# Optimization experiments

Hardware: AMD Instinct MI355X
Metric: run time of the kernel (lower is better)

## Reference

```python
import jax, jax.numpy as jnp
import numpy as np

L, B, S, D, H = 6, 2, 2048, 512, 8
DH = D // H
FF = 4 * D
EPS = 1e-5


def setup_inputs() -> dict:
    key = jax.random.key(0)
    ks = jax.random.split(key, 10)
    w = lambda k, shape: jax.random.normal(k, shape, jnp.float32) * 0.02
    return {
        "query": jax.random.normal(ks[0], (B, S, D), jnp.float32),
        "key": jax.random.normal(ks[1], (B, S, D), jnp.float32),
        "query_mask": jnp.ones((B, S), jnp.int32),
        "key_mask": jnp.ones((B, S), jnp.int32),
        # per-layer stacked params; conv1d(kernel=1) == linear with weight [out,in]
        "Wq": w(ks[2], (L, D, D)), "bq": jnp.zeros((L, D), jnp.float32),
        "Wk": w(ks[3], (L, D, D)), "bk": jnp.zeros((L, D), jnp.float32),
        "Wv": w(ks[4], (L, D, D)), "bv": jnp.zeros((L, D), jnp.float32),
        "Wo": w(ks[5], (L, D, D)), "bo": jnp.zeros((L, D), jnp.float32),
        "ln1_g": jnp.ones((L, D), jnp.float32), "ln1_b": jnp.zeros((L, D), jnp.float32),
        "ff_w1": w(ks[6], (L, FF, D)), "ff_b1": jnp.zeros((L, FF), jnp.float32),
        "ff_w2": w(ks[7], (L, D, FF)), "ff_b2": jnp.zeros((L, D), jnp.float32),
        "ln2_g": jnp.ones((L, D), jnp.float32), "ln2_b": jnp.zeros((L, D), jnp.float32),
    }


def _layer_norm(x, g, b):
    m = jnp.mean(x, axis=-1, keepdims=True)
    v = jnp.mean(jnp.square(x - m), axis=-1, keepdims=True)
    return (x - m) * jax.lax.rsqrt(v + EPS) * g + b


def reference(query, key, query_mask, key_mask,
              Wq, bq, Wk, bk, Wv, bv, Wo, bo,
              ln1_g, ln1_b, ff_w1, ff_b1, ff_w2, ff_b2, ln2_g, ln2_b):
    b_, s_, d_ = query.shape
    kpad = (key_mask == 0)[:, None, None, :]          # [B,1,1,K]
    qm = query_mask.astype(query.dtype)[:, :, None]    # [B,S,1]
    x = query
    for i in range(L):
        # QKV projections (conv1d kernel-size-1 == linear), split heads -> [B,H,S,DH]
        def split(t):
            return t.reshape(b_, s_, H, DH).transpose(0, 2, 1, 3)
        q = split(x @ Wq[i].T + bq[i]) * (float(DH) ** -0.5)
        k = split(key @ Wk[i].T + bk[i])
        v = split(key @ Wv[i].T + bv[i])
        attn = jnp.einsum('bhqd,bhkd->bhqk', q, k)
        attn = jnp.where(kpad, -jnp.inf, attn)
        attn = jax.nn.softmax(attn, axis=-1)
        o = jnp.einsum('bhqk,bhkd->bhqd', attn, v)
        o = o.transpose(0, 2, 1, 3).reshape(b_, s_, H * DH)
        o = (o @ Wo[i].T + bo[i]) * qm                 # output proj + query mask
        x = _layer_norm(o + x, ln1_g[i], ln1_b[i])
        h = jax.nn.leaky_relu(x @ ff_w1[i].T + ff_b1[i], 0.01)
        f = (h @ ff_w2[i].T + ff_b2[i]) * qm           # FFN mask on output
        x = _layer_norm(f + x, ln2_g[i], ln2_b[i])
    return x
```

## Files before the change

kernel.cpp:

```cpp
#include <hip/hip_runtime.h>
#include <stdint.h>

constexpr int LAYERS = 6;
constexpr int Bc = 2, Sc = 2048, Dc = 512, Hc = 8, DHc = 64, FFc = 2048;
constexpr int Mc = Bc * Sc;
constexpr int NS = 2;
constexpr int KCHUNK = Sc / NS;

typedef __attribute__((ext_vector_type(8))) __bf16 bf16x8;
typedef __attribute__((ext_vector_type(4))) __bf16 bf16x4;
typedef __attribute__((ext_vector_type(4))) float f32x4;

__device__ __forceinline__ void async_ld16(const void* g, void* lds) {
  __builtin_amdgcn_global_load_lds(
      (const __attribute__((address_space(1))) uint32_t*)g,
      (__attribute__((address_space(3))) uint32_t*)lds, 16, 0, 0);
}

__global__ __launch_bounds__(256) void cvt_kernel(const float* __restrict__ in,
                                                  __bf16* __restrict__ out, int n) {
  int i = (blockIdx.x * 256 + threadIdx.x) * 4;
  if (i + 4 > n) return;
  const float4 v = *(const float4*)(in + i);
  bf16x4 o;
  o[0] = (__bf16)v.x; o[1] = (__bf16)v.y; o[2] = (__bf16)v.z; o[3] = (__bf16)v.w;
  *(bf16x4*)(out + i) = o;
}

__global__ __launch_bounds__(256) void cvt_kv_kernel(const float* __restrict__ Wk,
                                                     const float* __restrict__ Wv,
                                                     __bf16* __restrict__ out) {
  size_t i = ((size_t)blockIdx.x * 256 + threadIdx.x) * 4;
  int n = (int)(i / ((size_t)Dc * Dc));
  int lyr = n >> 1, p = n & 1;
  size_t idx = i - (size_t)n * Dc * Dc;
  const float* src = (p ? Wv : Wk) + (size_t)lyr * Dc * Dc + idx;
  const float4 v = *(const float4*)src;
  bf16x4 o;
  o[0] = (__bf16)v.x; o[1] = (__bf16)v.y; o[2] = (__bf16)v.z; o[3] = (__bf16)v.w;
  *(bf16x4*)(out + i) = o;
}

__global__ __launch_bounds__(256) void kbias_kernel(const int* __restrict__ km,
                                                    float* __restrict__ kb, int n) {
  int i = blockIdx.x * 256 + threadIdx.x;
  if (i < n) kb[i] = km[i] ? 0.f : -1e30f;
}

template <int BM, int BN, int WM, int WN, int EPI>
__global__ __launch_bounds__(256) void gemm_bt(
    const __bf16* __restrict__ A, const __bf16* __restrict__ W,
    const float* __restrict__ bias, const float* __restrict__ bias2,
    float* __restrict__ outf, __bf16* __restrict__ outb,
    __bf16* __restrict__ outb2, float scale,
    int M, int N, int K, int Kstride) {
  constexpr int BK = 64;
  __shared__ __bf16 As[2][BM * BK];
  __shared__ __bf16 Bs[2][BN * BK];
  const int tid = threadIdx.x;
  const int l15 = tid & 15;
  const int lg = (tid & 63) >> 4;
  const int w = tid >> 6;
  const int wm = w >> 1, wn = w & 1;
  const int tm = blockIdx.y * BM;
  const int tn = blockIdx.x * BN;
  const int z = blockIdx.z;
  const __bf16* Ap = A + (size_t)tm * Kstride + (size_t)z * K;
  const __bf16* Wp = W + (size_t)tn * Kstride + (size_t)z * K;
  f32x4 acc[WM][WN] = {};

  auto stage = [&](int k0, int bf) {
#pragma unroll
    for (int c = 0; c < BM * 8 / 256; ++c) {
      int cc = c * 256 + tid;
      int r = cc >> 3, s = cc & 7;
      int ss = s ^ (r & 7);
      async_ld16(Ap + (size_t)r * Kstride + k0 + ss * 8, &As[bf][cc * 8]);
    }
#pragma unroll
    for (int c = 0; c < BN * 8 / 256; ++c) {
      int cc = c * 256 + tid;
      int r = cc >> 3, s = cc & 7;
      int ss = s ^ (r & 7);
      async_ld16(Wp + (size_t)r * Kstride + k0 + ss * 8, &Bs[bf][cc * 8]);
    }
  };

  const int nk = K / BK;
  stage(0, 0);
  __syncthreads();
  int buf = 0;
  for (int t = 0; t < nk; ++t) {
    if (t + 1 < nk) stage((t + 1) * BK, buf ^ 1);
    bf16x8 af[WM][2], bfr[WN][2];
#pragma unroll
    for (int i = 0; i < WM; ++i) {
      int row = wm * WM * 16 + i * 16 + l15;
#pragma unroll
      for (int kf = 0; kf < 2; ++kf)
        af[i][kf] = *(const bf16x8*)&As[buf][row * 64 + (((kf * 4 + lg) ^ (row & 7)) * 8)];
    }
#pragma unroll
    for (int j = 0; j < WN; ++j) {
      int row = wn * WN * 16 + j * 16 + l15;
#pragma unroll
      for (int kf = 0; kf < 2; ++kf)
        bfr[j][kf] = *(const bf16x8*)&Bs[buf][row * 64 + (((kf * 4 + lg) ^ (row & 7)) * 8)];
    }
#pragma unroll
    for (int kf = 0; kf < 2; ++kf)
#pragma unroll
      for (int i = 0; i < WM; ++i)
#pragma unroll
        for (int j = 0; j < WN; ++j)
          acc[i][j] = __builtin_amdgcn_mfma_f32_16x16x32_bf16(af[i][kf], bfr[j][kf], acc[i][j], 0, 0, 0);
    __syncthreads();
    buf ^= 1;
  }

  if constexpr (EPI == 6) {
    const bool isV = ((tn & 1023) >= 512);
    const int lyr = tn >> 10;
    const int b = tm >> 11;
    const int sbase = tm & (Sc - 1);
    if (isV) {
      __bf16* T = (__bf16*)&As[0][0];
#pragma unroll
      for (int i = 0; i < WM; ++i) {
#pragma unroll
        for (int j = 0; j < WN; ++j) {
          const int d = wn * WN * 16 + j * 16 + l15;
          const int dg = (tn & 511) + d;
          const float bv = bias2[lyr * 512 + dg];
          const int s0 = wm * WM * 16 + i * 16 + lg * 4;
          bf16x4 pk;
#pragma unroll
          for (int r = 0; r < 4; ++r) pk[r] = (__bf16)(acc[i][j][r] + bv);
          const int slot = (s0 >> 3) ^ (d & 7);
          *(bf16x4*)&T[d * 64 + slot * 8 + (s0 & 7)] = pk;
        }
      }
      __syncthreads();
      const int rr = tid >> 3;
      const int c8 = tid & 7;
#pragma unroll
      for (int pass = 0; pass < 4; ++pass) {
        const int d = pass * 32 + rr;
        const int slot = c8 ^ (d & 7);
        bf16x8 v8 = *(const bf16x8*)&T[d * 64 + slot * 8];
        const int dg = (tn & 511) + d;
        const int h = dg >> 6, dh = dg & 63;
        *(bf16x8*)&outb2[((((size_t)(lyr * Bc + b) * Hc + h)) * DHc + dh) * Sc +
                         sbase + c8 * 8] = v8;
      }
    } else {
#pragma unroll
      for (int i = 0; i < WM; ++i) {
#pragma unroll
        for (int j = 0; j < WN; ++j) {
          const int d = wn * WN * 16 + j * 16 + l15;
          const int dg = (tn & 511) + d;
          const float bv = bias[lyr * 512 + dg];
          const int h = dg >> 6, dh = dg & 63;
#pragma unroll
          for (int r = 0; r < 4; ++r) {
            const int s = sbase + wm * WM * 16 + i * 16 + lg * 4 + r;
            outb[((((size_t)(lyr * Bc + b) * Hc + h)) * Sc + s) * DHc + dh] =
                (__bf16)(acc[i][j][r] + bv);
          }
        }
      }
    }
    return;
  }

#pragma unroll
  for (int i = 0; i < WM; ++i) {
#pragma unroll
    for (int j = 0; j < WN; ++j) {
      const int n = tn + wn * WN * 16 + j * 16 + l15;
      float bv;
      if constexpr (EPI == 0) {
        bv = (z == 0) ? bias[n] : 0.f;
      } else {
        bv = bias[n];
      }
#pragma unroll
      for (int r = 0; r < 4; ++r) {
        const int m = tm + wm * WM * 16 + i * 16 + lg * 4 + r;
        float v = acc[i][j][r] + bv;
        if constexpr (EPI == 0) {
          outf[(size_t)z * M * N + (size_t)m * N + n] = v;
        } else if constexpr (EPI == 1) {
          int b = m >> 11, s = m & (Sc - 1);
          int h = n >> 6, dh = n & 63;
          outb[(((size_t)(b * Hc + h)) * Sc + s) * DHc + dh] = (__bf16)(v * scale);
        } else if constexpr (EPI == 4) {
          float lv = v > 0.f ? v : 0.01f * v;
          outb[(size_t)m * N + n] = (__bf16)lv;
        }
      }
    }
  }
}

__global__ __launch_bounds__(256, 4) void attn_kernel(
    const __bf16* __restrict__ q, const __bf16* __restrict__ k,
    const __bf16* __restrict__ vt, const float* __restrict__ kb,
    __bf16* __restrict__ Opart, float* __restrict__ mpart,
    float* __restrict__ lpart) {
  const int bid = blockIdx.x;
  const int o = (bid & 7) * 128 + (bid >> 3);
  const int qb = o & 31;
  const int p = o >> 5;
  const int bh = p >> 1;
  const int z = p & 1;
  const int b = bh >> 3;
  const int w = threadIdx.x >> 6;
  const int l = threadIdx.x & 63;
  const int l15 = l & 15;
  const int lg = l >> 4;
  const int tid = threadIdx.x;
  const int qbase = qb * 64 + w * 16;
  const int k0 = z * KCHUNK;

  const __bf16* qp = q + ((size_t)bh * Sc + qbase) * DHc;
  const __bf16* kp = k + (size_t)bh * Sc * DHc;
  const __bf16* vp = vt + (size_t)bh * DHc * Sc;
  const float* kbp = kb + (size_t)b * Sc;

  bf16x8 qf[2];
  qf[0] = *(const bf16x8*)(qp + l15 * DHc + lg * 8);
  qf[1] = *(const bf16x8*)(qp + l15 * DHc + 32 + lg * 8);

  bf16x8 onesf;
#pragma unroll
  for (int i = 0; i < 8; ++i) onesf[i] = (__bf16)1.0f;

  f32x4 oacc[4] = {};
  f32x4 lacc = {};
  float mr[4] = {-1e30f, -1e30f, -1e30f, -1e30f};

  __shared__ __bf16 Ks[2][4096];
  __shared__ __bf16 Vs[2][4096];
  __shared__ __bf16 P[4][1024];

  auto stage = [&](int t, int bf) {
    const int kt = k0 + t * 64;
#pragma unroll
    for (int ii = 0; ii < 2; ++ii) {
      int i = ii * 256 + tid;
      int r = i >> 3;
      int bsrc = (i & 7) ^ (r & 7);
      async_ld16(kp + (size_t)(kt + r) * DHc + bsrc * 8, &Ks[bf][i * 8]);
      async_ld16(vp + (size_t)r * Sc + kt + bsrc * 8, &Vs[bf][i * 8]);
    }
  };

  float mb[4];
#pragma unroll
  for (int cb = 0; cb < 4; ++cb) mb[cb] = kbp[k0 + cb * 16 + l15];
  stage(0, 0);
  __syncthreads();

  constexpr int NT = KCHUNK / 64;
  int buf = 0;
  for (int t = 0; t < NT; ++t) {
    const int kt = k0 + t * 64;
    if (t + 1 < NT) stage(t + 1, buf ^ 1);
    float mbn[4];
    if (t + 1 < NT) {
#pragma unroll
      for (int cb = 0; cb < 4; ++cb) mbn[cb] = kbp[kt + 64 + cb * 16 + l15];
    }

    f32x4 sacc[4] = {};
#pragma unroll
    for (int kf = 0; kf < 2; ++kf) {
#pragma unroll
      for (int cb = 0; cb < 4; ++cb) {
        int row = cb * 16 + l15;
        bf16x8 kfr = *(const bf16x8*)&Ks[buf][row * 64 + (((kf * 4 + lg) ^ (row & 7)) * 8)];
        sacc[cb] = __builtin_amdgcn_mfma_f32_16x16x32_bf16(qf[kf], kfr, sacc[cb], 0, 0, 0);
      }
    }
#pragma unroll
    for (int cb = 0; cb < 4; ++cb) {
#pragma unroll
      for (int j = 0; j < 4; ++j) sacc[cb][j] += mb[cb];
    }
    float mx[4];
#pragma unroll
    for (int j = 0; j < 4; ++j) {
      float m0 = fmaxf(fmaxf(sacc[0][j], sacc[1][j]), fmaxf(sacc[2][j], sacc[3][j]));
#pragma unroll
      for (int d = 1; d < 16; d <<= 1) m0 = fmaxf(m0, __shfl_xor(m0, d, 64));
      mx[j] = m0;
    }
    bool need = (mx[0] > mr[0] + 8.f) || (mx[1] > mr[1] + 8.f) ||
                (mx[2] > mr[2] + 8.f) || (mx[3] > mr[3] + 8.f);
    if (__any(need)) {
#pragma unroll
      for (int j = 0; j < 4; ++j) {
        float mn = fmaxf(mr[j], mx[j]);
        float f = __expf(mr[j] - mn);
        mr[j] = mn;
        lacc[j] *= f;
#pragma unroll
        for (int db = 0; db < 4; ++db) oacc[db][j] *= f;
      }
    }
#pragma unroll
    for (int cb = 0; cb < 4; ++cb)
#pragma unroll
      for (int j = 0; j < 4; ++j) sacc[cb][j] = __expf(sacc[cb][j] - mr[j]);

#pragma unroll
    for (int cb = 0; cb < 4; ++cb)
#pragma unroll
      for (int j = 0; j < 4; ++j) {
        int qrow = lg * 4 + j;
        P[w][qrow * 64 + ((cb * 16 + l15) ^ ((qrow & 7) << 3))] = (__bf16)sacc[cb][j];
      }
#pragma unroll
    for (int kf = 0; kf < 2; ++kf) {
      bf16x8 pf = *(const bf16x8*)&P[w][l15 * 64 + (((kf * 4 + lg) ^ (l15 & 7)) * 8)];
      lacc = __builtin_amdgcn_mfma_f32_16x16x32_bf16(pf, onesf, lacc, 0, 0, 0);
#pragma unroll
      for (int db = 0; db < 4; ++db) {
        int row = db * 16 + l15;
        bf16x8 vf = *(const bf16x8*)&Vs[buf][row * 64 + (((kf * 4 + lg) ^ (row & 7)) * 8)];
        oacc[db] = __builtin_amdgcn_mfma_f32_16x16x32_bf16(pf, vf, oacc[db], 0, 0, 0);
      }
    }
    if (t + 1 < NT) {
#pragma unroll
      for (int cb = 0; cb < 4; ++cb) mb[cb] = mbn[cb];
    }
    __syncthreads();
    buf ^= 1;
  }

  const size_t obase = (((size_t)(z * Bc * Hc + bh)) * Sc + qbase) * DHc;
#pragma unroll
  for (int db = 0; db < 4; ++db)
#pragma unroll
    for (int j = 0; j < 4; ++j)
      Opart[obase + (size_t)(lg * 4 + j) * DHc + db * 16 + l15] = (__bf16)oacc[db][j];
  if (l15 == 0) {
#pragma unroll
    for (int j = 0; j < 4; ++j) {
      int row = (z * Bc * Hc + bh) * Sc + qbase + lg * 4 + j;
      mpart[row] = mr[j];
      lpart[row] = lacc[j];
    }
  }
}

__global__ __launch_bounds__(256) void attn_combine(
    const __bf16* __restrict__ Opart, const float* __restrict__ mpart,
    const float* __restrict__ lpart, __bf16* __restrict__ out) {
  int t = blockIdx.x * 256 + threadIdx.x;
  int d = t & 63;
  int row = t >> 6;
  int bh = row >> 11, s = row & (Sc - 1);
  constexpr int RSTRIDE = Bc * Hc * Sc;
  float m0 = mpart[row], m1 = mpart[RSTRIDE + row];
  float l0 = lpart[row], l1 = lpart[RSTRIDE + row];
  float M = fmaxf(m0, m1);
  float e0 = __expf(m0 - M), e1 = __expf(m1 - M);
  float denom = e0 * l0 + e1 * l1;
  float o0 = (float)Opart[(size_t)row * DHc + d];
  float o1 = (float)Opart[((size_t)RSTRIDE + row) * DHc + d];
  float o = (e0 * o0 + e1 * o1) / denom;
  int b = bh >> 3, h = bh & 7;
  out[(((size_t)b * Sc + s)) * Dc + h * DHc + d] = (__bf16)o;
}

__global__ __launch_bounds__(256) void add_ln_kernel(
    const float* __restrict__ res, const float* __restrict__ res2,
    const int* __restrict__ rmask, const float* __restrict__ xin,
    const float* __restrict__ g, const float* __restrict__ bb,
    float* __restrict__ xo, __bf16* __restrict__ xbo) {
  const int row = blockIdx.x;
  const int tid = threadIdx.x;
  const float* rp = res + (size_t)row * Dc;
  const float* xp = xin + (size_t)row * Dc;
  float mfac = rmask ? (float)rmask[row] : 1.f;
  float a0 = rp[tid], a1 = rp[tid + 256];
  if (res2) {
    const float* r2p = res2 + (size_t)row * Dc;
    a0 += r2p[tid];
    a1 += r2p[tid + 256];
  }
  float v0 = a0 * mfac + xp[tid];
  float v1 = a1 * mfac + xp[tid + 256];
  float s = v0 + v1;
#pragma unroll
  for (int d = 1; d < 64; d <<= 1) s += __shfl_xor(s, d, 64);
  __shared__ float red[4], red2[4];
  if ((tid & 63) == 0) red[tid >> 6] = s;
  __syncthreads();
  float mean = (red[0] + red[1] + red[2] + red[3]) * (1.0f / Dc);
  float d0 = v0 - mean, d1 = v1 - mean;
  float qq = d0 * d0 + d1 * d1;
#pragma unroll
  for (int d = 1; d < 64; d <<= 1) qq += __shfl_xor(qq, d, 64);
  if ((tid & 63) == 0) red2[tid >> 6] = qq;
  __syncthreads();
  float var = (red2[0] + red2[1] + red2[2] + red2[3]) * (1.0f / Dc);
  float rs = rsqrtf(var + 1e-5f);
  float o0 = d0 * rs * g[tid] + bb[tid];
  float o1 = d1 * rs * g[tid + 256] + bb[tid + 256];
  xo[(size_t)row * Dc + tid] = o0;
  xo[(size_t)row * Dc + tid + 256] = o1;
  xbo[(size_t)row * Dc + tid] = (__bf16)o0;
  xbo[(size_t)row * Dc + tid + 256] = (__bf16)o1;
}

extern "C" void kernel_launch(void* const* d_in, const int* in_sizes, int n_in,
                              void* d_out, int out_size, void* d_ws, size_t ws_size,
                              hipStream_t stream) {
  (void)in_sizes; (void)n_in; (void)out_size; (void)ws_size;
  const float* query = (const float*)d_in[0];
  const float* key   = (const float*)d_in[1];
  const int* qmask   = (const int*)d_in[2];
  const int* kmask   = (const int*)d_in[3];
  const float* Wq = (const float*)d_in[4];
  const float* bq = (const float*)d_in[5];
  const float* Wk = (const float*)d_in[6];
  const float* bk = (const float*)d_in[7];
  const float* Wv = (const float*)d_in[8];
  const float* bv = (const float*)d_in[9];
  const float* Wo = (const float*)d_in[10];
  const float* bo = (const float*)d_in[11];
  const float* ln1g = (const float*)d_in[12];
  const float* ln1b = (const float*)d_in[13];
  const float* fw1 = (const float*)d_in[14];
  const float* fb1 = (const float*)d_in[15];
  const float* fw2 = (const float*)d_in[16];
  const float* fb2 = (const float*)d_in[17];
  const float* ln2g = (const float*)d_in[18];
  const float* ln2b = (const float*)d_in[19];

  char* ws = (char*)d_ws;
  size_t off = 0;
  auto carve = [&](size_t bytes) -> void* {
    void* p = ws + off;
    off += (bytes + 255) & ~(size_t)255;
    return p;
  };
  float* x_f    = (float*)carve((size_t)Mc * Dc * 4);
  float* tmp_f  = (float*)carve((size_t)2 * Mc * Dc * 4);
  __bf16* x_b   = (__bf16*)carve((size_t)Mc * Dc * 2);
  __bf16* key_b = (__bf16*)carve((size_t)Mc * Dc * 2);
  __bf16* q_b   = (__bf16*)carve((size_t)Mc * Dc * 2);
  __bf16* at_b  = (__bf16*)carve((size_t)Mc * Dc * 2);
  __bf16* h_b   = (__bf16*)carve((size_t)Mc * FFc * 2);
  __bf16* k_all = (__bf16*)carve((size_t)LAYERS * Mc * Dc * 2);
  __bf16* vt_all= (__bf16*)carve((size_t)LAYERS * Mc * Dc * 2);
  __bf16* wq_b  = (__bf16*)carve((size_t)LAYERS * Dc * Dc * 2);
  __bf16* wkv_b = (__bf16*)carve((size_t)LAYERS * 2 * Dc * Dc * 2);
  __bf16* wo_b  = (__bf16*)carve((size_t)LAYERS * Dc * Dc * 2);
  __bf16* w1_b  = (__bf16*)carve((size_t)LAYERS * FFc * Dc * 2);
  __bf16* w2_b  = (__bf16*)carve((size_t)LAYERS * Dc * FFc * 2);
  float* ml_f   = (float*)carve((size_t)NS * Bc * Hc * Sc * 4 * 2);
  float* kb_f   = (float*)carve((size_t)Bc * Sc * 4);

  __bf16* opart_b = h_b;
  float* mpart_f = ml_f;
  float* lpart_f = ml_f + (size_t)NS * Bc * Hc * Sc;
  float* tmp2_f = tmp_f + (size_t)Mc * Dc;

  auto cvt = [&](const float* src, __bf16* dst, int n) {
    cvt_kernel<<<n / 1024, 256, 0, stream>>>(src, dst, n);
  };
  cvt(query, x_b, Mc * Dc);
  cvt(key, key_b, Mc * Dc);
  cvt(Wq, wq_b, LAYERS * Dc * Dc);
  cvt_kv_kernel<<<LAYERS * 2 * Dc * Dc / 1024, 256, 0, stream>>>(Wk, Wv, wkv_b);
  cvt(Wo, wo_b, LAYERS * Dc * Dc);
  cvt(fw1, w1_b, LAYERS * FFc * Dc);
  cvt(fw2, w2_b, LAYERS * Dc * FFc);
  kbias_kernel<<<Bc * Sc / 256, 256, 0, stream>>>(kmask, kb_f, Bc * Sc);
  hipMemcpyAsync(x_f, query, (size_t)Mc * Dc * 4, hipMemcpyDeviceToDevice, stream);

  const dim3 blk(256);
  const dim3 gP64(Dc / 64, Mc / 64);
  const dim3 gOP(Dc / 64, Mc / 64, 2);
  const dim3 gFF2(Dc / 64, Mc / 64, 2);
  const dim3 gKV(LAYERS * 2 * Dc / 128, Mc / 64);
  const dim3 gFF1(FFc / 64, Mc / 64);
  const dim3 gAttn(Sc / 64 * Bc * Hc * NS);
  const dim3 gComb(Bc * Hc * Sc * DHc / 256);

  gemm_bt<64, 128, 2, 4, 6><<<gKV, blk, 0, stream>>>(
      key_b, wkv_b, bk, bv, nullptr, k_all, vt_all, 1.0f,
      Mc, LAYERS * 2 * Dc, Dc, Dc);

  for (int i = 0; i < LAYERS; ++i) {
    const __bf16* wq_i = wq_b + (size_t)i * Dc * Dc;
    const __bf16* wo_i = wo_b + (size_t)i * Dc * Dc;
    const __bf16* w1_i = w1_b + (size_t)i * FFc * Dc;
    const __bf16* w2_i = w2_b + (size_t)i * Dc * FFc;
    const __bf16* k_i  = k_all + (size_t)i * Mc * Dc;
    const __bf16* vt_i = vt_all + (size_t)i * Mc * Dc;

    gemm_bt<64, 64, 2, 2, 1><<<gP64, blk, 0, stream>>>(
        x_b, wq_i, bq + i * Dc, nullptr, nullptr, q_b, nullptr, 0.125f,
        Mc, Dc, Dc, Dc);
    attn_kernel<<<gAttn, blk, 0, stream>>>(q_b, k_i, vt_i, kb_f,
                                           opart_b, mpart_f, lpart_f);
    attn_combine<<<gComb, blk, 0, stream>>>(opart_b, mpart_f, lpart_f, at_b);
    gemm_bt<64, 64, 2, 2, 0><<<gOP, blk, 0, stream>>>(
        at_b, wo_i, bo + i * Dc, nullptr, tmp_f, nullptr, nullptr, 1.0f,
        Mc, Dc, Dc / 2, Dc);
    add_ln_kernel<<<Mc, blk, 0, stream>>>(tmp_f, tmp2_f, qmask, x_f,
                                          ln1g + i * Dc, ln1b + i * Dc, x_f, x_b);
    gemm_bt<64, 64, 2, 2, 4><<<gFF1, blk, 0, stream>>>(
        x_b, w1_i, fb1 + i * FFc, nullptr, nullptr, h_b, nullptr, 1.0f,
        Mc, FFc, Dc, Dc);
    gemm_bt<64, 64, 2, 2, 0><<<gFF2, blk, 0, stream>>>(
        h_b, w2_i, fb2 + i * Dc, nullptr, tmp_f, nullptr, nullptr, 1.0f,
        Mc, Dc, FFc / 2, FFc);
    add_ln_kernel<<<Mc, blk, 0, stream>>>(tmp_f, tmp2_f, qmask, x_f,
                                          ln2g + i * Dc, ln2b + i * Dc, x_f, x_b);
  }
  hipMemcpyAsync(d_out, x_f, (size_t)Mc * Dc * 4, hipMemcpyDeviceToDevice, stream);
}
```

Baseline: 841.2 us.

## Transpose QK MFMA so P stays in registers, drop LDS P buffer

The attention kernel swaps the MFMA operands for QK^T so each lane holds scores for a single query row. That makes the row max a two-step cross-lane reduction with one scalar running max per lane. The probability tile is rebuilt as MFMA A-operands through cross-lane shuffles instead of a round trip through the shared-memory P buffer, and the key-mask bias is read per tile as float4. Launch bounds rise to 5 waves, and the FFN1 GEMM moves to 64x128 tiles. The cost is extra shuffle instructions and more register pressure from the higher occupancy target.

```diff
diff --git a/kernel.cpp b/kernel.cpp
--- a/kernel.cpp
+++ b/kernel.cpp
@@ -204,7 +204,7 @@
   }
 }
 
-__global__ __launch_bounds__(256, 4) void attn_kernel(
+__global__ __launch_bounds__(256, 5) void attn_kernel(
     const __bf16* __restrict__ q, const __bf16* __restrict__ k,
     const __bf16* __restrict__ vt, const float* __restrict__ kb,
     __bf16* __restrict__ Opart, float* __restrict__ mpart,
@@ -239,11 +239,10 @@
 
   f32x4 oacc[4] = {};
   f32x4 lacc = {};
-  float mr[4] = {-1e30f, -1e30f, -1e30f, -1e30f};
+  float mr = -1e30f;
 
   __shared__ __bf16 Ks[2][4096];
   __shared__ __bf16 Vs[2][4096];
-  __shared__ __bf16 P[4][1024];
 
   auto stage = [&](int t, int bf) {
     const int kt = k0 + t * 64;
@@ -257,9 +256,6 @@
     }
   };
 
-  float mb[4];
-#pragma unroll
-  for (int cb = 0; cb < 4; ++cb) mb[cb] = kbp[k0 + cb * 16 + l15];
   stage(0, 0);
   __syncthreads();
 
@@ -268,11 +264,11 @@
   for (int t = 0; t < NT; ++t) {
     const int kt = k0 + t * 64;
     if (t + 1 < NT) stage(t + 1, buf ^ 1);
-    float mbn[4];
-    if (t + 1 < NT) {
-#pragma unroll
-      for (int cb = 0; cb < 4; ++cb) mbn[cb] = kbp[kt + 64 + cb * 16 + l15];
-    }
+
+    float4 mb4[4];
+#pragma unroll
+    for (int cb = 0; cb < 4; ++cb)
+      mb4[cb] = *(const float4*)&kbp[kt + cb * 16 + lg * 4];
 
     f32x4 sacc[4] = {};
 #pragma unroll
@@ -281,61 +277,74 @@
       for (int cb = 0; cb < 4; ++cb) {
         int row = cb * 16 + l15;
         bf16x8 kfr = *(const bf16x8*)&Ks[buf][row * 64 + (((kf * 4 + lg) ^ (row & 7)) * 8)];
-        sacc[cb] = __builtin_amdgcn_mfma_f32_16x16x32_bf16(qf[kf], kfr, sacc[cb], 0, 0, 0);
-      }
-    }
+        sacc[cb] = __builtin_amdgcn_mfma_f32_16x16x32_bf16(kfr, qf[kf], sacc[cb], 0, 0, 0);
+      }
+    }
+    sacc[0][0] += mb4[0].x; sacc[0][1] += mb4[0].y; sacc[0][2] += mb4[0].z; sacc[0][3] += mb4[0].w;
+    sacc[1][0] += mb4[1].x; sacc[1][1] += mb4[1].y; sacc[1][2] += mb4[1].z; sacc[1][3] += mb4[1].w;
+    sacc[2][0] += mb4[2].x; sacc[2][1] += mb4[2].y; sacc[2][2] += mb4[2].z; sacc[2][3] += mb4[2].w;
+    sacc[3][0] += mb4[3].x; sacc[3][1] += mb4[3].y; sacc[3][2] += mb4[3].z; sacc[3][3] += mb4[3].w;
+
+    float mx = sacc[0][0];
+#pragma unroll
+    for (int cb = 0; cb < 4; ++cb)
+#pragma unroll
+      for (int r = 0; r < 4; ++r) mx = fmaxf(mx, sacc[cb][r]);
+    mx = fmaxf(mx, __shfl_xor(mx, 16, 64));
+    mx = fmaxf(mx, __shfl_xor(mx, 32, 64));
+
+    if (__any(mx > mr + 8.f)) {
+      float mn = fmaxf(mr, mx);
+      float f = __expf(mr - mn);
+      mr = mn;
+      float fj[4];
+#pragma unroll
+      for (int j = 0; j < 4; ++j) fj[j] = __shfl(f, lg * 4 + j, 64);
+#pragma unroll
+      for (int j = 0; j < 4; ++j) lacc[j] *= fj[j];
+#pragma unroll
+      for (int db = 0; db < 4; ++db)
+#pragma unroll
+        for (int j = 0; j < 4; ++j) oacc[db][j] *= fj[j];
+    }
+
+    unsigned pw[4][2];
 #pragma unroll
     for (int cb = 0; cb < 4; ++cb) {
 #pragma unroll
-      for (int j = 0; j < 4; ++j) sacc[cb][j] += mb[cb];
-    }
-    float mx[4];
-#pragma unroll
-    for (int j = 0; j < 4; ++j) {
-      float m0 = fmaxf(fmaxf(sacc[0][j], sacc[1][j]), fmaxf(sacc[2][j], sacc[3][j]));
-#pragma unroll
-      for (int d = 1; d < 16; d <<= 1) m0 = fmaxf(m0, __shfl_xor(m0, d, 64));
-      mx[j] = m0;
-    }
-    bool need = (mx[0] > mr[0] + 8.f) || (mx[1] > mr[1] + 8.f) ||
-                (mx[2] > mr[2] + 8.f) || (mx[3] > mr[3] + 8.f);
-    if (__any(need)) {
-#pragma unroll
-      for (int j = 0; j < 4; ++j) {
-        float mn = fmaxf(mr[j], mx[j]);
-        float f = __expf(mr[j] - mn);
-        mr[j] = mn;
-        lacc[j] *= f;
-#pragma unroll
-        for (int db = 0; db < 4; ++db) oacc[db][j] *= f;
-      }
-    }
-#pragma unroll
-    for (int cb = 0; cb < 4; ++cb)
-#pragma unroll
-      for (int j = 0; j < 4; ++j) sacc[cb][j] = __expf(sacc[cb][j] - mr[j]);
-
-#pragma unroll
-    for (int cb = 0; cb < 4; ++cb)
-#pragma unroll
-      for (int j = 0; j < 4; ++j) {
-        int qrow = lg * 4 + j;
-        P[w][qrow * 64 + ((cb * 16 + l15) ^ ((qrow & 7) << 3))] = (__bf16)sacc[cb][j];
-      }
+      for (int w2 = 0; w2 < 2; ++w2) {
+        union { __bf16 h[2]; unsigned u; } cu;
+        cu.h[0] = (__bf16)__expf(sacc[cb][2 * w2] - mr);
+        cu.h[1] = (__bf16)__expf(sacc[cb][2 * w2 + 1] - mr);
+        pw[cb][w2] = cu.u;
+      }
+    }
+
+    const int srcA = ((lg & 1) * 2) * 16 + l15;
+    const int srcB = srcA + 16;
+    const bool hi = (lg >> 1) & 1;
 #pragma unroll
     for (int kf = 0; kf < 2; ++kf) {
-      bf16x8 pf = *(const bf16x8*)&P[w][l15 * 64 + (((kf * 4 + lg) ^ (l15 & 7)) * 8)];
-      lacc = __builtin_amdgcn_mfma_f32_16x16x32_bf16(pf, onesf, lacc, 0, 0, 0);
+      unsigned t0a = __shfl((int)pw[kf * 2][0], srcA, 64);
+      unsigned t0b = __shfl((int)pw[kf * 2 + 1][0], srcA, 64);
+      unsigned t1a = __shfl((int)pw[kf * 2][1], srcA, 64);
+      unsigned t1b = __shfl((int)pw[kf * 2 + 1][1], srcA, 64);
+      unsigned t2a = __shfl((int)pw[kf * 2][0], srcB, 64);
+      unsigned t2b = __shfl((int)pw[kf * 2 + 1][0], srcB, 64);
+      unsigned t3a = __shfl((int)pw[kf * 2][1], srcB, 64);
+      unsigned t3b = __shfl((int)pw[kf * 2 + 1][1], srcB, 64);
+      union { unsigned u[4]; bf16x8 v; } pa;
+      pa.u[0] = hi ? t0b : t0a;
+      pa.u[1] = hi ? t1b : t1a;
+      pa.u[2] = hi ? t2b : t2a;
+      pa.u[3] = hi ? t3b : t3a;
+      lacc = __builtin_amdgcn_mfma_f32_16x16x32_bf16(pa.v, onesf, lacc, 0, 0, 0);
 #pragma unroll
       for (int db = 0; db < 4; ++db) {
         int row = db * 16 + l15;
         bf16x8 vf = *(const bf16x8*)&Vs[buf][row * 64 + (((kf * 4 + lg) ^ (row & 7)) * 8)];
-        oacc[db] = __builtin_amdgcn_mfma_f32_16x16x32_bf16(pf, vf, oacc[db], 0, 0, 0);
-      }
-    }
-    if (t + 1 < NT) {
-#pragma unroll
-      for (int cb = 0; cb < 4; ++cb) mb[cb] = mbn[cb];
+        oacc[db] = __builtin_amdgcn_mfma_f32_16x16x32_bf16(pa.v, vf, oacc[db], 0, 0, 0);
+      }
     }
     __syncthreads();
     buf ^= 1;
@@ -347,13 +356,11 @@
 #pragma unroll
     for (int j = 0; j < 4; ++j)
       Opart[obase + (size_t)(lg * 4 + j) * DHc + db * 16 + l15] = (__bf16)oacc[db][j];
+  const int row0 = (z * Bc * Hc + bh) * Sc + qbase;
+  if (lg == 0) mpart[row0 + l15] = mr;
   if (l15 == 0) {
 #pragma unroll
-    for (int j = 0; j < 4; ++j) {
-      int row = (z * Bc * Hc + bh) * Sc + qbase + lg * 4 + j;
-      mpart[row] = mr[j];
-      lpart[row] = lacc[j];
-    }
+    for (int j = 0; j < 4; ++j) lpart[row0 + lg * 4 + j] = lacc[j];
   }
 }
 
@@ -490,7 +497,7 @@
   const dim3 gOP(Dc / 64, Mc / 64, 2);
   const dim3 gFF2(Dc / 64, Mc / 64, 2);
   const dim3 gKV(LAYERS * 2 * Dc / 128, Mc / 64);
-  const dim3 gFF1(FFc / 64, Mc / 64);
+  const dim3 gFF1(FFc / 128, Mc / 64);
   const dim3 gAttn(Sc / 64 * Bc * Hc * NS);
   const dim3 gComb(Bc * Hc * Sc * DHc / 256);
 
@@ -517,7 +524,7 @@
         Mc, Dc, Dc / 2, Dc);
     add_ln_kernel<<<Mc, blk, 0, stream>>>(tmp_f, tmp2_f, qmask, x_f,
                                           ln1g + i * Dc, ln1b + i * Dc, x_f, x_b);
-    gemm_bt<64, 64, 2, 2, 4><<<gFF1, blk, 0, stream>>>(
+    gemm_bt<64, 128, 2, 4, 4><<<gFF1, blk, 0, stream>>>(
         x_b, w1_i, fb1 + i * FFc, nullptr, nullptr, h_b, nullptr, 1.0f,
         Mc, FFc, Dc, Dc);
     gemm_bt<64, 64, 2, 2, 0><<<gFF2, blk, 0, stream>>>(
```

Measured after the change: 815.4 us. 3.1% less time.
